# Kernel optimization log

Hardware: AMD Instinct MI355X
Metric: run time of the kernel (lower is better)

Reference implementation:

```python
import jax, jax.numpy as jnp
import numpy as np

BINS = 32
MAX_DIST = 128
EMB = 1024
DQ = 64
DV = 64
H = 16
B = 8
L = 1024


def _t5_bucket_table():
    # matches: clamp(n,max=m) + (log(clamp(n,min=m)-m+1)*(bins-1-m)/log(max_distance-m+1)).long()
    n = np.arange(MAX_DIST + 1)
    m = BINS // 2
    idx = np.minimum(n, m) + (
        np.log(np.maximum(n, m) - m + 1) * (BINS - 1 - m) / np.log(MAX_DIST - m + 1)
    ).astype(np.int64)
    return jnp.asarray(idx)


def setup_inputs() -> dict:
    key = jax.random.key(0)
    ks = jax.random.split(key, 8)
    s = 0.02
    return {
        "x": jax.random.normal(ks[0], (B, L, EMB), dtype=jnp.float32),
        "qk_w": jax.random.normal(ks[1], (2 * DQ * H, EMB), dtype=jnp.float32) * s,
        "qk_b": jnp.zeros((2 * DQ * H,), dtype=jnp.float32),
        "v_w": jax.random.normal(ks[2], (DV * H, EMB), dtype=jnp.float32) * s,
        "v_b": jnp.zeros((DV * H,), dtype=jnp.float32),
        "out_w": jax.random.normal(ks[3], (EMB, DV * H), dtype=jnp.float32) * s,
        "out_b": jnp.zeros((EMB,), dtype=jnp.float32),
        "bias": jax.random.normal(ks[4], (BINS, H), dtype=jnp.float32) * s,  # causal -> bins rows
    }


def reference(x, qk_w, qk_b, v_w, v_b, out_w, out_b, bias):
    # projections
    qk = (x @ qk_w.T + qk_b).reshape(B, L, H, 2 * DQ).transpose(0, 2, 1, 3)  # [B,H,L,2DQ]
    q, k = qk[..., :DQ], qk[..., DQ:]
    v = (x @ v_w.T + v_b).reshape(B, L, H, DV).transpose(0, 2, 1, 3)  # [B,H,L,DV]

    # T5 relative-position bias (causal): gather per (i-j) distance bucket
    idx_tab = _t5_bucket_table()
    shifts = jnp.arange(L)[:, None] - jnp.arange(L)[None, :]  # [L,L], i - j
    bins_idx = idx_tab[jnp.clip(jnp.abs(shifts), 0, MAX_DIST)]  # [L,L]
    bmat = bias[bins_idx].transpose(2, 0, 1)  # [H,L,L]
    bmat = jnp.where(shifts < 0, -jnp.inf, bmat)  # causal mask (j > i)

    scale = 1.0 / np.sqrt(DQ).astype(np.float32)
    scores = jnp.einsum("bhid,bhjd->bhij", q, k) * scale + bmat  # [B,H,L,L]
    attn = jax.nn.softmax(scores, axis=-1)
    out = jnp.einsum("bhij,bhjd->bhid", attn, v)  # [B,H,L,DV]
    out = out.transpose(0, 2, 1, 3).reshape(B, L, H * DV)
    return out @ out_w.T + out_b
```

## Files before the change

kernel.cpp:

```cpp
#include <hip/hip_runtime.h>
#include <cmath>


typedef _Float16 f16x8 __attribute__((ext_vector_type(8)));
typedef _Float16 f16x4 __attribute__((ext_vector_type(4)));
typedef float    f32x4 __attribute__((ext_vector_type(4)));

#define NEG_INF (-__builtin_inff())
#define LOG2E 1.4426950408889634f

#if __has_builtin(__builtin_amdgcn_exp2f)
#define EXP2(x) __builtin_amdgcn_exp2f(x)
#else
#define EXP2(x) exp2f(x)
#endif

__device__ __forceinline__ void gl_lds16(const void* g, void* l) {
  __builtin_amdgcn_global_load_lds(
      (__attribute__((address_space(1))) void*)g,
      (__attribute__((address_space(3))) void*)l,
      16, 0, 0);
}

__device__ __forceinline__ f32x4 mfma32(f16x8 a, f16x8 b, f32x4 c) {
  return __builtin_amdgcn_mfma_f32_16x16x32_f16(a, b, c, 0, 0, 0);
}
__device__ __forceinline__ f32x4 mfma16(f16x4 a, f16x4 b, f32x4 c) {
  return __builtin_amdgcn_mfma_f32_16x16x16f16(a, b, c, 0, 0, 0);
}

typedef __attribute__((address_space(3))) _Float16* lds_f16p;

__global__ void cvt_kernel(const float* __restrict__ in,
                           _Float16* __restrict__ out, int n4) {
  int i = blockIdx.x * blockDim.x + threadIdx.x;
  if (i >= n4) return;
  float4 v = reinterpret_cast<const float4*>(in)[i];
  f16x4 o;
  o[0] = (_Float16)v.x; o[1] = (_Float16)v.y;
  o[2] = (_Float16)v.z; o[3] = (_Float16)v.w;
  reinterpret_cast<f16x4*>(out)[i] = o;
}

#define GEMM_VM8 asm volatile("s_waitcnt vmcnt(8)" ::: "memory")
#define GEMM_VM4 asm volatile("s_waitcnt vmcnt(4)" ::: "memory")
#define GEMM_VM0 asm volatile("s_waitcnt vmcnt(0)" ::: "memory")
#define GEMM_BAR __builtin_amdgcn_s_barrier()
#define DSR(d, a, o) \
  asm volatile("ds_read_b128 %0, %1 offset:" o : "=v"(d) : "v"(a))

#define GEMM_STAGE(buf, kk)                         \
  do {                                              \
    gl_lds16(pA0 + (kk), &lds_a[buf][wofs]);        \
    gl_lds16(pA1 + (kk), &lds_a[buf][2048 + wofs]); \
    gl_lds16(pB0 + (kk), &lds_b[buf][wofs]);        \
    gl_lds16(pB1 + (kk), &lds_b[buf][2048 + wofs]); \
  } while (0)

#define GEMM_COMPUTE(aB, bB)                             \
  do {                                                   \
    f16x8 af0, af1, af2, af3, bf0, bf1, bf2, bf3;        \
    DSR(af0, aB, "0");                                   \
    DSR(bf0, bB, "0");                                   \
    DSR(af1, aB, "1024");                                \
    DSR(bf1, bB, "1024");                                \
    DSR(af2, aB, "2048");                                \
    DSR(bf2, bB, "2048");                                \
    DSR(af3, aB, "3072");                                \
    DSR(bf3, bB, "3072");                                \
    asm volatile("s_waitcnt lgkmcnt(4)" ::: "memory");   \
    __builtin_amdgcn_sched_barrier(0);                   \
    __builtin_amdgcn_s_setprio(1);                       \
    acc[0][0] = mfma32(af0, bf0, acc[0][0]);             \
    acc[0][1] = mfma32(af0, bf1, acc[0][1]);             \
    acc[1][0] = mfma32(af1, bf0, acc[1][0]);             \
    acc[1][1] = mfma32(af1, bf1, acc[1][1]);             \
    asm volatile("s_waitcnt lgkmcnt(0)" ::: "memory");   \
    __builtin_amdgcn_sched_barrier(0);                   \
    acc[0][2] = mfma32(af0, bf2, acc[0][2]);             \
    acc[0][3] = mfma32(af0, bf3, acc[0][3]);             \
    acc[1][2] = mfma32(af1, bf2, acc[1][2]);             \
    acc[1][3] = mfma32(af1, bf3, acc[1][3]);             \
    acc[2][0] = mfma32(af2, bf0, acc[2][0]);             \
    acc[2][1] = mfma32(af2, bf1, acc[2][1]);             \
    acc[2][2] = mfma32(af2, bf2, acc[2][2]);             \
    acc[2][3] = mfma32(af2, bf3, acc[2][3]);             \
    acc[3][0] = mfma32(af3, bf0, acc[3][0]);             \
    acc[3][1] = mfma32(af3, bf1, acc[3][1]);             \
    acc[3][2] = mfma32(af3, bf2, acc[3][2]);             \
    acc[3][3] = mfma32(af3, bf3, acc[3][3]);             \
    __builtin_amdgcn_s_setprio(0);                       \
  } while (0)

template <int MODE>
__global__ __launch_bounds__(256, 3) void gemm_kernel(
    const _Float16* __restrict__ A, const _Float16* __restrict__ Bm,
    int M, int N, int K,
    const float* __restrict__ bias_q, const float* __restrict__ bias_v,
    _Float16* __restrict__ qkbuf, _Float16* __restrict__ vtbuf,
    const float* __restrict__ bias_o, float* __restrict__ outf) {
  __shared__ __align__(16) _Float16 lds_a[3][128 * 32];
  __shared__ __align__(16) _Float16 lds_b[3][128 * 32];
  const int t = threadIdx.x;
  const int w = t >> 6;
  const int lane = t & 63;
  const int lq = lane & 15, lg = lane >> 4;
  const int wr = w >> 1, wc = w & 1;
  const int m0 = blockIdx.y * 128, n0 = blockIdx.x * 128;

  const int stc = ((t & 3) ^ ((t >> 3) & 3)) * 8;
  const _Float16* pA0 = A + (size_t)(m0 + (t >> 2)) * K + stc;
  const _Float16* pA1 = pA0 + (size_t)64 * K;
  const _Float16* pB0 = Bm + (size_t)(n0 + (t >> 2)) * K + stc;
  const _Float16* pB1 = pB0 + (size_t)64 * K;
  const int wofs = w * 512;

  const int xsw = (lq >> 1) & 3;
  const uint32_t aB0 = (uint32_t)(uintptr_t)(lds_f16p)&lds_a[0][0] +
                       (uint32_t)((wr * 64 + lq) * 64 + ((lg ^ xsw) << 4));
  const uint32_t aB1 = aB0 + 8192;
  const uint32_t aB2 = aB0 + 16384;
  const uint32_t bB0 = (uint32_t)(uintptr_t)(lds_f16p)&lds_b[0][0] +
                       (uint32_t)((wc * 64 + lq) * 64 + ((lg ^ xsw) << 4));
  const uint32_t bB1 = bB0 + 8192;
  const uint32_t bB2 = bB0 + 16384;

  f32x4 acc[4][4];
#pragma unroll
  for (int mi = 0; mi < 4; ++mi)
#pragma unroll
    for (int ni = 0; ni < 4; ++ni) acc[mi][ni] = (f32x4){0.f, 0.f, 0.f, 0.f};

  GEMM_STAGE(0, 0);
  GEMM_STAGE(1, 32);
  for (int kt = 0; kt + 160 <= K; kt += 96) {
    GEMM_STAGE(2, kt + 64);
    GEMM_VM8;
    GEMM_BAR;
    GEMM_COMPUTE(aB0, bB0);
    GEMM_BAR;
    GEMM_STAGE(0, kt + 96);
    GEMM_VM8;
    GEMM_BAR;
    GEMM_COMPUTE(aB1, bB1);
    GEMM_BAR;
    GEMM_STAGE(1, kt + 128);
    GEMM_VM8;
    GEMM_BAR;
    GEMM_COMPUTE(aB2, bB2);
    GEMM_BAR;
  }
  GEMM_VM4;
  GEMM_BAR;
  GEMM_COMPUTE(aB0, bB0);
  GEMM_BAR;
  GEMM_VM0;
  GEMM_BAR;
  GEMM_COMPUTE(aB1, bB1);

  if (MODE == 0) {
    const bool isqk = (n0 < 2048);
#pragma unroll
    for (int mi = 0; mi < 4; ++mi)
#pragma unroll
      for (int ni = 0; ni < 4; ++ni)
#pragma unroll
        for (int r = 0; r < 4; ++r) {
          const int mg = m0 + wr * 64 + mi * 16 + lg * 4 + r;
          const int ng = n0 + wc * 64 + ni * 16 + lq;
          const int bb = mg >> 10, ii = mg & 1023;
          float val = acc[mi][ni][r];
          if (isqk) {
            val += bias_q[ng];
            const int hh = ng >> 7, cc = ng & 127;
            qkbuf[((size_t)((bb * 16 + hh) * 1024 + ii)) * 128 + cc] =
                (_Float16)val;
          } else {
            const int nn = ng - 2048;
            val += bias_v[nn];
            const int hh = nn >> 6, dv = nn & 63;
            vtbuf[((size_t)((bb * 16 + hh) * 64 + dv)) * 1024 + ii] =
                (_Float16)val;
          }
        }
  } else {
#pragma unroll
    for (int mi = 0; mi < 4; ++mi)
#pragma unroll
      for (int ni = 0; ni < 4; ++ni)
#pragma unroll
        for (int r = 0; r < 4; ++r) {
          const int mg = m0 + wr * 64 + mi * 16 + lg * 4 + r;
          const int ng = n0 + wc * 64 + ni * 16 + lq;
          outf[(size_t)mg * N + ng] = acc[mi][ni][r] + bias_o[ng];
        }
  }
}

__device__ __forceinline__ void stage_kv(const _Float16* __restrict__ kb,
                                         const _Float16* __restrict__ vtb,
                                         int j0, _Float16* kl, _Float16* vl,
                                         int t) {
  const int r0 = t >> 3, c0 = t & 7;
  const int r1 = r0 + 32;
  const int kc0 = c0 ^ (r0 & 7), kc1 = c0 ^ (r1 & 7);
  gl_lds16(kb + (size_t)(j0 + r0) * 128 + kc0 * 8, kl + t * 8);
  gl_lds16(kb + (size_t)(j0 + r1) * 128 + kc1 * 8, kl + (t + 256) * 8);
  gl_lds16(vtb + (size_t)r0 * 1024 + j0 + kc0 * 8, vl + t * 8);
  gl_lds16(vtb + (size_t)r1 * 1024 + j0 + kc1 * 8, vl + (t + 256) * 8);
}

__device__ __forceinline__ void softmax16(f32x4 (&st)[4], f16x4 (&ph)[4],
                                          int qi, int j0, bool far,
                                          const float* __restrict__ tab,
                                          float t128, int lg4, float& m_run,
                                          float& l_part, f32x4 (&oacc)[4]) {
  float xs[16];
  float lmax = NEG_INF;
  if (far) {
#pragma unroll
    for (int js = 0; js < 4; ++js)
#pragma unroll
      for (int r = 0; r < 4; ++r) {
        const float xv = fmaf(st[js][r], 0.125f * LOG2E, t128);
        xs[js * 4 + r] = xv;
        lmax = fmaxf(lmax, xv);
      }
  } else {
#pragma unroll
    for (int js = 0; js < 4; ++js)
#pragma unroll
      for (int r = 0; r < 4; ++r) {
        const int jj = j0 + js * 16 + lg4 + r;
        const int dd = qi - jj;
        const int idx = dd < 0 ? 0 : (dd > 128 ? 128 : dd);
        const float xv =
            (dd < 0) ? NEG_INF : fmaf(st[js][r], 0.125f * LOG2E, tab[idx]);
        xs[js * 4 + r] = xv;
        lmax = fmaxf(lmax, xv);
      }
  }
  if (__any(lmax > m_run + 8.0f)) {
    float tmax = fmaxf(lmax, __shfl_xor(lmax, 16));
    tmax = fmaxf(tmax, __shfl_xor(tmax, 32));
    const float m_new = fmaxf(m_run, tmax);
    const float sf = EXP2(m_run - m_new);
    m_run = m_new;
    l_part *= sf;
    f32x4 sfv;
#pragma unroll
    for (int r = 0; r < 4; ++r) sfv[r] = __shfl(sf, lg4 + r);
#pragma unroll
    for (int db = 0; db < 4; ++db) oacc[db] *= sfv;
  }
  float ls = 0.f;
#pragma unroll
  for (int js = 0; js < 4; ++js)
#pragma unroll
    for (int r = 0; r < 4; ++r) {
      const float p = EXP2(xs[js * 4 + r] - m_run);
      ls += p;
      ph[js][r] = (_Float16)p;
    }
  l_part += ls;
}

__global__ __launch_bounds__(256, 4) void attn_kernel(
    const _Float16* __restrict__ qk,
    const _Float16* __restrict__ vt,
    const float* __restrict__ bias,
    _Float16* __restrict__ ao) {
  __shared__ __align__(16) _Float16 kls[2][64 * 64];
  __shared__ __align__(16) _Float16 vls[2][64 * 64];
  __shared__ float tab[132];
  const int t = threadIdx.x;
  const int bid = blockIdx.x;
  const int bh = (bid & 7) * 16 + (bid >> 6);
  const int b4 = (bid >> 3) & 7;
  const int h = bh & 15, b = bh >> 4;
  if (t < 129) {
    const int bucket =
        (t <= 16) ? t : 16 + (int)(log((double)(t - 15)) * 15.0 / log(113.0));
    tab[t] = bias[bucket * 16 + h] * LOG2E;
  }

  const int w = t >> 6, lane = t & 63;
  const int lq = lane & 15, lg = lane >> 4;
  const int lg4 = lg * 4, lg8 = lg * 8;
  const int tA = b4, tB = 15 - b4;
  const int q0A = tA * 64 + w * 16, q0B = tB * 64 + w * 16;
  const int qA = q0A + lq, qB = q0B + lq;
  const _Float16* qkb = qk + (size_t)bh * 1024 * 128;
  const _Float16* kb = qkb + 64;
  const _Float16* vtb = vt + (size_t)bh * 64 * 1024;

  const f16x8 qfA0 = *(const f16x8*)&qkb[qA * 128 + lg8];
  const f16x8 qfA1 = *(const f16x8*)&qkb[qA * 128 + 32 + lg8];
  const f16x8 qfB0 = *(const f16x8*)&qkb[qB * 128 + lg8];
  const f16x8 qfB1 = *(const f16x8*)&qkb[qB * 128 + 32 + lg8];

  f32x4 oA[4], oB[4];
#pragma unroll
  for (int db = 0; db < 4; ++db) {
    oA[db] = (f32x4){0.f, 0.f, 0.f, 0.f};
    oB[db] = (f32x4){0.f, 0.f, 0.f, 0.f};
  }
  float mA = NEG_INF, lAp = 0.f, mB = NEG_INF, lBp = 0.f;

  stage_kv(kb, vtb, 0, kls[0], vls[0], t);
  __syncthreads();
  const float t128 = tab[128];
  const int krsw = lq & 7;
  const int vsw = (lq & 7) << 1;
  int cur = 0;

  for (int jt = 0; jt <= tB; ++jt) {
    const int j0 = jt * 64;
    if (jt < tB) stage_kv(kb, vtb, j0 + 64, kls[cur ^ 1], vls[cur ^ 1], t);
    const bool aact = (jt <= tA);
    const _Float16* kbf = kls[cur];
    const _Float16* vbf = vls[cur];

    f32x4 stA[4], stB[4];
#pragma unroll
    for (int js = 0; js < 4; ++js) {
      const int rowb = (js * 16 + lq) * 64;
      const f16x8 kf0 = *(const f16x8*)&kbf[rowb + ((lg ^ krsw) << 3)];
      const f16x8 kf1 = *(const f16x8*)&kbf[rowb + (((lg + 4) ^ krsw) << 3)];
      if (aact) {
        stA[js] = mfma32(kf0, qfA0, (f32x4){0.f, 0.f, 0.f, 0.f});
        stA[js] = mfma32(kf1, qfA1, stA[js]);
      }
      stB[js] = mfma32(kf0, qfB0, (f32x4){0.f, 0.f, 0.f, 0.f});
      stB[js] = mfma32(kf1, qfB1, stB[js]);
    }

    f16x4 phA[4], phB[4];
    if (aact)
      softmax16(stA, phA, qA, j0, q0A - j0 >= 192, tab, t128, lg4, mA, lAp,
                oA);
    softmax16(stB, phB, qB, j0, q0B - j0 >= 192, tab, t128, lg4, mB, lBp, oB);

#pragma unroll
    for (int js = 0; js < 4; ++js)
#pragma unroll
      for (int db = 0; db < 4; ++db) {
        const f16x4 vf = *(const f16x4*)&vbf[(db * 16 + lq) * 64 +
                                             ((((js << 2) + lg) ^ vsw) << 2)];
        if (aact) oA[db] = mfma16(phA[js], vf, oA[db]);
        oB[db] = mfma16(phB[js], vf, oB[db]);
      }

    __syncthreads();
    cur ^= 1;
  }

  _Float16* aob = ao + ((size_t)b * 1024) * 1024 + h * 64;
  {
    float lt = lAp + __shfl_xor(lAp, 16);
    lt += __shfl_xor(lt, 32);
    f32x4 linv;
#pragma unroll
    for (int r = 0; r < 4; ++r) linv[r] = 1.0f / __shfl(lt, lg4 + r);
#pragma unroll
    for (int db = 0; db < 4; ++db)
#pragma unroll
      for (int r = 0; r < 4; ++r)
        aob[(size_t)(q0A + lg4 + r) * 1024 + db * 16 + lq] =
            (_Float16)(oA[db][r] * linv[r]);
  }
  {
    float lt = lBp + __shfl_xor(lBp, 16);
    lt += __shfl_xor(lt, 32);
    f32x4 linv;
#pragma unroll
    for (int r = 0; r < 4; ++r) linv[r] = 1.0f / __shfl(lt, lg4 + r);
#pragma unroll
    for (int db = 0; db < 4; ++db)
#pragma unroll
      for (int r = 0; r < 4; ++r)
        aob[(size_t)(q0B + lg4 + r) * 1024 + db * 16 + lq] =
            (_Float16)(oB[db][r] * linv[r]);
  }
}

extern "C" void kernel_launch(void* const* d_in, const int* in_sizes, int n_in,
                              void* d_out, int out_size, void* d_ws,
                              size_t ws_size, hipStream_t stream) {
  const float* x = (const float*)d_in[0];
  const float* qk_w = (const float*)d_in[1];
  const float* qk_b = (const float*)d_in[2];
  const float* v_w = (const float*)d_in[3];
  const float* v_b = (const float*)d_in[4];
  const float* out_w = (const float*)d_in[5];
  const float* out_b = (const float*)d_in[6];
  const float* bias = (const float*)d_in[7];
  float* out = (float*)d_out;

  _Float16* xb = (_Float16*)d_ws;
  _Float16* wb = xb + (size_t)8388608;
  _Float16* owb = wb + (size_t)3145728;
  _Float16* qkbuf = owb + (size_t)1048576;
  _Float16* vtbuf = qkbuf + (size_t)16777216;
  _Float16* ao = vtbuf + (size_t)8388608;

  cvt_kernel<<<8192, 256, 0, stream>>>(x, xb, 2097152);
  cvt_kernel<<<2048, 256, 0, stream>>>(qk_w, wb, 524288);
  cvt_kernel<<<1024, 256, 0, stream>>>(v_w, wb + 2097152, 262144);
  cvt_kernel<<<1024, 256, 0, stream>>>(out_w, owb, 262144);

  gemm_kernel<0><<<dim3(24, 64), 256, 0, stream>>>(
      xb, wb, 8192, 3072, 1024, qk_b, v_b, qkbuf, vtbuf, nullptr, nullptr);

  attn_kernel<<<1024, 256, 0, stream>>>(qkbuf, vtbuf, bias, ao);

  gemm_kernel<1><<<dim3(8, 64), 256, 0, stream>>>(
      ao, owb, 8192, 1024, 1024, nullptr, nullptr, nullptr, nullptr, out_b, out);
}
```

Baseline: 185.2 us.

## Merge convert launches and hand-schedule LDS reads in attention loop

Replaces the four fp32-to-fp16 conversion launches with one kernel that routes by block index. In the attention loop, K and V fragments are loaded from LDS with explicit ds_read instructions on precomputed swizzled addresses. The V reads are issued before the softmax so their latency overlaps it. Waits become explicit vmcnt/lgkmcnt counts with raw barriers instead of __syncthreads, and s_setprio raises priority around the MFMA blocks. This relies on the vmcnt(4) count matching the number of loads stage_kv issues, and it adds register pressure from holding 16 V fragments.

```diff
diff --git a/kernel.cpp b/kernel.cpp
--- a/kernel.cpp
+++ b/kernel.cpp
@@ -31,23 +31,44 @@
 
 typedef __attribute__((address_space(3))) _Float16* lds_f16p;
 
-__global__ void cvt_kernel(const float* __restrict__ in,
-                           _Float16* __restrict__ out, int n4) {
-  int i = blockIdx.x * blockDim.x + threadIdx.x;
-  if (i >= n4) return;
-  float4 v = reinterpret_cast<const float4*>(in)[i];
+#define DSR(d, a, o) \
+  asm volatile("ds_read_b128 %0, %1 offset:" o : "=v"(d) : "v"(a))
+#define DSR64(d, a, o) \
+  asm volatile("ds_read_b64 %0, %1 offset:" o : "=v"(d) : "v"(a))
+#define LGKM0                                          \
+  asm volatile("s_waitcnt lgkmcnt(0)" ::: "memory");   \
+  __builtin_amdgcn_sched_barrier(0)
+
+__global__ void cvt4_kernel(const float* __restrict__ x,
+                            const float* __restrict__ w1,
+                            const float* __restrict__ w2,
+                            const float* __restrict__ w3,
+                            _Float16* __restrict__ ox, _Float16* __restrict__ o1,
+                            _Float16* __restrict__ o2, _Float16* __restrict__ o3) {
+  const int bid = blockIdx.x;
+  const float* src;
+  _Float16* dst;
+  int idx;
+  if (bid < 8192) {
+    src = x; dst = ox; idx = bid * 256 + threadIdx.x;
+  } else if (bid < 10240) {
+    src = w1; dst = o1; idx = (bid - 8192) * 256 + threadIdx.x;
+  } else if (bid < 11264) {
+    src = w2; dst = o2; idx = (bid - 10240) * 256 + threadIdx.x;
+  } else {
+    src = w3; dst = o3; idx = (bid - 11264) * 256 + threadIdx.x;
+  }
+  float4 v = reinterpret_cast<const float4*>(src)[idx];
   f16x4 o;
   o[0] = (_Float16)v.x; o[1] = (_Float16)v.y;
   o[2] = (_Float16)v.z; o[3] = (_Float16)v.w;
-  reinterpret_cast<f16x4*>(out)[i] = o;
+  reinterpret_cast<f16x4*>(dst)[idx] = o;
 }
 
 #define GEMM_VM8 asm volatile("s_waitcnt vmcnt(8)" ::: "memory")
 #define GEMM_VM4 asm volatile("s_waitcnt vmcnt(4)" ::: "memory")
 #define GEMM_VM0 asm volatile("s_waitcnt vmcnt(0)" ::: "memory")
 #define GEMM_BAR __builtin_amdgcn_s_barrier()
-#define DSR(d, a, o) \
-  asm volatile("ds_read_b128 %0, %1 offset:" o : "=v"(d) : "v"(a))
 
 #define GEMM_STAGE(buf, kk)                         \
   do {                                              \
@@ -312,28 +333,73 @@
   const float t128 = tab[128];
   const int krsw = lq & 7;
   const int vsw = (lq & 7) << 1;
+
+  const uint32_t kbase = (uint32_t)(uintptr_t)(lds_f16p)&kls[0][0];
+  const uint32_t vbase = (uint32_t)(uintptr_t)(lds_f16p)&vls[0][0];
+  const uint32_t ka0b = kbase + (uint32_t)(lq * 128 + ((lg ^ krsw) << 4));
+  const uint32_t ka1b = kbase + (uint32_t)(lq * 128 + (((lg + 4) ^ krsw) << 4));
+  const uint32_t va0b = vbase + (uint32_t)(lq * 128 + ((lg ^ vsw) << 3));
+  const uint32_t va1b = vbase + (uint32_t)(lq * 128 + (((4 + lg) ^ vsw) << 3));
+  const uint32_t va2b = vbase + (uint32_t)(lq * 128 + (((8 + lg) ^ vsw) << 3));
+  const uint32_t va3b = vbase + (uint32_t)(lq * 128 + (((12 + lg) ^ vsw) << 3));
+
   int cur = 0;
-
   for (int jt = 0; jt <= tB; ++jt) {
     const int j0 = jt * 64;
-    if (jt < tB) stage_kv(kb, vtb, j0 + 64, kls[cur ^ 1], vls[cur ^ 1], t);
+    if (jt < tB) {
+      stage_kv(kb, vtb, j0 + 64, kls[cur ^ 1], vls[cur ^ 1], t);
+      asm volatile("s_waitcnt vmcnt(4)" ::: "memory");
+    } else {
+      asm volatile("s_waitcnt vmcnt(0)" ::: "memory");
+    }
+    __builtin_amdgcn_s_barrier();
     const bool aact = (jt <= tA);
-    const _Float16* kbf = kls[cur];
-    const _Float16* vbf = vls[cur];
+    const uint32_t co = cur ? 8192u : 0u;
+    const uint32_t ka0 = ka0b + co, ka1 = ka1b + co;
+    const uint32_t va0 = va0b + co, va1 = va1b + co, va2 = va2b + co,
+                   va3 = va3b + co;
+
+    f16x8 kf0[4], kf1[4];
+    DSR(kf0[0], ka0, "0");
+    DSR(kf1[0], ka1, "0");
+    DSR(kf0[1], ka0, "2048");
+    DSR(kf1[1], ka1, "2048");
+    DSR(kf0[2], ka0, "4096");
+    DSR(kf1[2], ka1, "4096");
+    DSR(kf0[3], ka0, "6144");
+    DSR(kf1[3], ka1, "6144");
+    LGKM0;
 
     f32x4 stA[4], stB[4];
+    __builtin_amdgcn_s_setprio(1);
 #pragma unroll
     for (int js = 0; js < 4; ++js) {
-      const int rowb = (js * 16 + lq) * 64;
-      const f16x8 kf0 = *(const f16x8*)&kbf[rowb + ((lg ^ krsw) << 3)];
-      const f16x8 kf1 = *(const f16x8*)&kbf[rowb + (((lg + 4) ^ krsw) << 3)];
       if (aact) {
-        stA[js] = mfma32(kf0, qfA0, (f32x4){0.f, 0.f, 0.f, 0.f});
-        stA[js] = mfma32(kf1, qfA1, stA[js]);
+        stA[js] = mfma32(kf0[js], qfA0, (f32x4){0.f, 0.f, 0.f, 0.f});
+        stA[js] = mfma32(kf1[js], qfA1, stA[js]);
       }
-      stB[js] = mfma32(kf0, qfB0, (f32x4){0.f, 0.f, 0.f, 0.f});
-      stB[js] = mfma32(kf1, qfB1, stB[js]);
+      stB[js] = mfma32(kf0[js], qfB0, (f32x4){0.f, 0.f, 0.f, 0.f});
+      stB[js] = mfma32(kf1[js], qfB1, stB[js]);
     }
+    __builtin_amdgcn_s_setprio(0);
+
+    f16x4 vf[4][4];
+    DSR64(vf[0][0], va0, "0");
+    DSR64(vf[0][1], va0, "2048");
+    DSR64(vf[0][2], va0, "4096");
+    DSR64(vf[0][3], va0, "6144");
+    DSR64(vf[1][0], va1, "0");
+    DSR64(vf[1][1], va1, "2048");
+    DSR64(vf[1][2], va1, "4096");
+    DSR64(vf[1][3], va1, "6144");
+    DSR64(vf[2][0], va2, "0");
+    DSR64(vf[2][1], va2, "2048");
+    DSR64(vf[2][2], va2, "4096");
+    DSR64(vf[2][3], va2, "6144");
+    DSR64(vf[3][0], va3, "0");
+    DSR64(vf[3][1], va3, "2048");
+    DSR64(vf[3][2], va3, "4096");
+    DSR64(vf[3][3], va3, "6144");
 
     f16x4 phA[4], phB[4];
     if (aact)
@@ -341,17 +407,18 @@
                 oA);
     softmax16(stB, phB, qB, j0, q0B - j0 >= 192, tab, t128, lg4, mB, lBp, oB);
 
+    LGKM0;
+    __builtin_amdgcn_s_setprio(1);
 #pragma unroll
     for (int js = 0; js < 4; ++js)
 #pragma unroll
       for (int db = 0; db < 4; ++db) {
-        const f16x4 vf = *(const f16x4*)&vbf[(db * 16 + lq) * 64 +
-                                             ((((js << 2) + lg) ^ vsw) << 2)];
-        if (aact) oA[db] = mfma16(phA[js], vf, oA[db]);
-        oB[db] = mfma16(phB[js], vf, oB[db]);
+        if (aact) oA[db] = mfma16(phA[js], vf[js][db], oA[db]);
+        oB[db] = mfma16(phB[js], vf[js][db], oB[db]);
       }
-
-    __syncthreads();
+    __builtin_amdgcn_s_setprio(0);
+
+    __builtin_amdgcn_s_barrier();
     cur ^= 1;
   }
 
@@ -404,10 +471,8 @@
   _Float16* vtbuf = qkbuf + (size_t)16777216;
   _Float16* ao = vtbuf + (size_t)8388608;
 
-  cvt_kernel<<<8192, 256, 0, stream>>>(x, xb, 2097152);
-  cvt_kernel<<<2048, 256, 0, stream>>>(qk_w, wb, 524288);
-  cvt_kernel<<<1024, 256, 0, stream>>>(v_w, wb + 2097152, 262144);
-  cvt_kernel<<<1024, 256, 0, stream>>>(out_w, owb, 262144);
+  cvt4_kernel<<<12288, 256, 0, stream>>>(x, qk_w, v_w, out_w, xb, wb,
+                                         wb + 2097152, owb);
 
   gemm_kernel<0><<<dim3(24, 64), 256, 0, stream>>>(
       xb, wb, 8192, 3072, 1024, qk_b, v_b, qkbuf, vtbuf, nullptr, nullptr);
```

Measured after the change: 223.1 us. 1.21x slower.
